# Kernel tuning notes

Hardware: AMD Instinct MI355X
Metric: run time of the kernel (lower is better)

Reference implementation:

```python
import jax, jax.numpy as jnp
import numpy as np
from math import factorial, sqrt

BATCH = 4096
RS_IN = [(16, 0), (16, 1), (16, 2)]   # (mul, l), parity 0
RS_OUT = [(16, 0), (16, 1), (16, 2)]

# selection rule: l_filter in [|l_in-l_out|, l_in+l_out]
SET_LF = sorted({l for (_, li) in RS_IN for (_, lo) in RS_OUT
                 for l in range(abs(li - lo), li + lo + 1)})
Y_OFF = {l: sum(2 * k + 1 for k in SET_LF if k < l) for l in SET_LF}
Y_DIM = sum(2 * l + 1 for l in SET_LF)  # 25


def wigner_3j(j1, j2, j3, m1, m2, m3):
    if m1 + m2 + m3 != 0 or not (abs(j1 - j2) <= j3 <= j1 + j2):
        return 0.0
    if abs(m1) > j1 or abs(m2) > j2 or abs(m3) > j3:
        return 0.0
    f = factorial
    pre = sqrt(f(j1 + j2 - j3) * f(j1 - j2 + j3) * f(-j1 + j2 + j3) / f(j1 + j2 + j3 + 1))
    pre *= sqrt(f(j1 + m1) * f(j1 - m1) * f(j2 + m2) * f(j2 - m2) * f(j3 + m3) * f(j3 - m3))
    s = 0.0
    for t in range(max(0, j2 - j3 - m1, j1 - j3 + m2),
                   min(j1 + j2 - j3, j1 - m1, j2 + m2) + 1):
        s += (-1) ** t / (f(t) * f(j3 - j2 + m1 + t) * f(j3 - j1 - m2 + t)
                          * f(j1 + j2 - j3 - t) * f(j1 - m1 - t) * f(j2 + m2 - t))
    return (-1) ** (j1 - j2 - m3) * pre * s


def real_to_complex(l):
    # A[M+l, m+l]: complex Y^M expressed in the real SH basis
    A = np.zeros((2 * l + 1, 2 * l + 1), dtype=np.complex128)
    A[l, l] = 1.0
    s2 = 1.0 / np.sqrt(2.0)
    for m in range(1, l + 1):
        A[l + m, l + m] = (-1) ** m * s2
        A[l + m, l - m] = 1j * (-1) ** m * s2
        A[l - m, l + m] = s2
        A[l - m, l - m] = -1j * s2
    return A


def clebsch_gordan(l1, l2, l3):
    # real, unit-Frobenius-norm invariant 3-tensor (unique up to sign)
    T = np.zeros((2 * l1 + 1, 2 * l2 + 1, 2 * l3 + 1))
    for m1 in range(-l1, l1 + 1):
        for m2 in range(-l2, l2 + 1):
            m3 = -(m1 + m2)
            if abs(m3) <= l3:
                T[m1 + l1, m2 + l2, m3 + l3] = wigner_3j(l1, l2, l3, m1, m2, m3)
    A1, A2, A3 = real_to_complex(l1), real_to_complex(l2), real_to_complex(l3)
    C = np.einsum('abc,ai,bj,ck->ijk', T, A1.conj(), A2.conj(), A3.conj())
    C = C.real if np.linalg.norm(C.real) >= np.linalg.norm(C.imag) else C.imag
    n = np.linalg.norm(C)
    return (C / n).astype(np.float32) if n > 0 else C.astype(np.float32)


# precompute per-block padded CG tensors and R offsets
R_OFF = {}
C_BLOCKS = {}
_off = 0
for _i, (_mo, _lo) in enumerate(RS_OUT):
    for _j, (_mi, _li) in enumerate(RS_IN):
        _lfs = list(range(abs(_li - _lo), _li + _lo + 1))
        R_OFF[(_i, _j)] = (_off, len(_lfs))
        _off += _mo * _mi * len(_lfs)
        _C = np.zeros((len(_lfs), 2 * _lo + 1, 2 * _li + 1, Y_DIM), dtype=np.float32)
        for _k, _lf in enumerate(_lfs):
            _o = Y_OFF[_lf]
            _C[_k, :, :, _o:_o + 2 * _lf + 1] = clebsch_gordan(_lo, _li, _lf)
        C_BLOCKS[(_i, _j)] = jnp.asarray(_C)
N_PATH = _off  # 4864


def setup_inputs() -> dict:
    key = jax.random.key(0)
    k1, k2, k3 = jax.random.split(key, 3)
    Y = jax.random.normal(k1, (Y_DIM, BATCH), dtype=jnp.float32)
    R = jax.random.normal(k2, (BATCH, N_PATH), dtype=jnp.float32)
    norm_coef = jax.random.uniform(k3, (len(RS_OUT), len(RS_IN), BATCH),
                                   dtype=jnp.float32, minval=0.5, maxval=1.5)
    return {"Y": Y, "R": R, "norm_coef": norm_coef}


def reference(Y, R, norm_coef):
    # Y: [Y_DIM, batch], R: [batch, N_PATH], norm_coef: [3, 3, batch]
    batch = Y.shape[1]
    rows = []
    for i, (mo, lo) in enumerate(RS_OUT):
        row = []
        for j, (mi, li) in enumerate(RS_IN):
            off, nlf = R_OFF[(i, j)]
            sub_R = R[:, off:off + mo * mi * nlf].reshape(batch, mo, mi, nlf)
            # fuse the per-l_filter loop into one contraction over k and m
            K = jnp.einsum('kijm,mz,zuvk,z->zuivj',
                           C_BLOCKS[(i, j)], Y, sub_R, norm_coef[i, j])
            row.append(K.reshape(batch, mo * (2 * lo + 1), mi * (2 * li + 1)))
        rows.append(jnp.concatenate(row, axis=2))
    return jnp.concatenate(rows, axis=1)  # [batch, 144, 144]
```

## Files before the change

kernel.cpp:

```cpp
#include <hip/hip_runtime.h>

#define NPATH 4864
#define YDIM  25
#define NW    259
#define NCG   1225


struct Tables {
    float cg[NCG];
    int   woff[NW];
    int   wlf[NW];
    int   wij[NW];
};

constexpr double cfact(int n) { double f = 1.0; for (int i = 2; i <= n; ++i) f *= (double)i; return f; }

constexpr double csqrt_(double x) {
    if (x <= 0.0) return 0.0;
    double g = x > 1.0 ? x : 1.0, p = 0.0;
    for (int it = 0; it < 200; ++it) { p = g; g = 0.5 * (g + x / g); if (g == p) break; }
    return g;
}
constexpr int cabs_(int x) { return x < 0 ? -x : x; }
constexpr int cmax3(int a, int b, int c) { int m = a > b ? a : b; return m > c ? m : c; }
constexpr int cmin3(int a, int b, int c) { int m = a < b ? a : b; return m < c ? m : c; }

constexpr double cwig3j(int j1, int j2, int j3, int m1, int m2, int m3) {
    if (m1 + m2 + m3 != 0) return 0.0;
    if (cabs_(m1) > j1 || cabs_(m2) > j2 || cabs_(m3) > j3) return 0.0;
    if (j3 < cabs_(j1 - j2) || j3 > j1 + j2) return 0.0;
    double prod = cfact(j1 + j2 - j3) * cfact(j1 - j2 + j3) * cfact(-j1 + j2 + j3)
                / cfact(j1 + j2 + j3 + 1);
    prod *= cfact(j1 + m1) * cfact(j1 - m1) * cfact(j2 + m2) * cfact(j2 - m2)
          * cfact(j3 + m3) * cfact(j3 - m3);
    double pre = csqrt_(prod);
    int t0 = cmax3(0, j2 - j3 - m1, j1 - j3 + m2);
    int t1 = cmin3(j1 + j2 - j3, j1 - m1, j2 + m2);
    double s = 0.0;
    for (int t = t0; t <= t1; ++t) {
        double d = cfact(t) * cfact(j3 - j2 + m1 + t) * cfact(j3 - j1 - m2 + t)
                 * cfact(j1 + j2 - j3 - t) * cfact(j1 - m1 - t) * cfact(j2 + m2 - t);
        s += ((t & 1) ? -1.0 : 1.0) / d;
    }
    int p = j1 - j2 - m3; p = ((p % 2) + 2) % 2;
    return (p ? -1.0 : 1.0) * pre * s;
}

struct Ent { int col; double re; double im; };

constexpr int arow(int l, int a, Ent* e) {
    int m = a - l;
    double s2 = csqrt_(0.5);
    if (m == 0) { e[0] = Ent{l, 1.0, 0.0}; return 1; }
    if (m > 0) {
        double sgn = (m & 1) ? -1.0 : 1.0;
        e[0] = Ent{l + m, sgn * s2, 0.0};
        e[1] = Ent{l - m, 0.0, sgn * s2};
        return 2;
    }
    int mm = -m;
    e[0] = Ent{l + mm, s2, 0.0};
    e[1] = Ent{l - mm, 0.0, -s2};
    return 2;
}

constexpr Tables make_tables() {
    Tables T{};
    const int CL1[19]  = {0,0,0,1,1,1,1,1,1,1,2,2,2,2,2,2,2,2,2};
    const int CL2[19]  = {0,1,2,0,1,1,1,2,2,2,0,1,1,1,2,2,2,2,2};
    const int CL3[19]  = {0,1,2,1,0,1,2,1,2,3,2,1,2,3,0,1,2,3,4};
    const int COFF[19] = {0,1,10,35,44,53,80,125,170,245,350,375,420,495,600,625,700,825,1000};

    for (int c = 0; c < 19; ++c) {
        int l1 = CL1[c], l2 = CL2[c], l3 = CL3[c], coff = COFF[c];
        int n1 = 2 * l1 + 1, n2 = 2 * l2 + 1, n3 = 2 * l3 + 1, ntot = n1 * n2 * n3;
        double Cre[225] = {}, Cim[225] = {};
        for (int a = 0; a < n1; ++a)
            for (int b = 0; b < n2; ++b) {
                int m1 = a - l1, m2 = b - l2, m3 = -(m1 + m2);
                if (cabs_(m3) > l3) continue;
                double tv = cwig3j(l1, l2, l3, m1, m2, m3);
                if (tv == 0.0) continue;
                int crow = m3 + l3;
                Ent e1[2] = {}, e2[2] = {}, e3[2] = {};
                int k1 = arow(l1, a, e1), k2 = arow(l2, b, e2), k3 = arow(l3, crow, e3);
                for (int x = 0; x < k1; ++x)
                    for (int y = 0; y < k2; ++y)
                        for (int w = 0; w < k3; ++w) {
                            double r1 = e1[x].re, i1 = -e1[x].im;
                            double r2 = e2[y].re, i2 = -e2[y].im;
                            double r3 = e3[w].re, i3 = -e3[w].im;
                            double pr = r1 * r2 - i1 * i2, pi = r1 * i2 + i1 * r2;
                            double qr = pr * r3 - pi * i3, qi = pr * i3 + pi * r3;
                            int idx = (e1[x].col * n2 + e2[y].col) * n3 + e3[w].col;
                            Cre[idx] += tv * qr;
                            Cim[idx] += tv * qi;
                        }
            }
        double sR = 0.0, sI = 0.0;
        for (int i = 0; i < ntot; ++i) { sR += Cre[i] * Cre[i]; sI += Cim[i] * Cim[i]; }
        bool useRe = (sR >= sI);
        double nn = csqrt_(useRe ? sR : sI);
        double inv = nn > 0.0 ? 1.0 / nn : 0.0;
        for (int i = 0; i < ntot; ++i)
            T.cg[coff + i] = (float)((useRe ? Cre[i] : Cim[i]) * inv);
    }

    const int NLFt[9]   = {1,1,1,1,3,3,1,3,5};
    const int CGOFF9[9] = {0,1,10,35,44,125,350,375,600};
    int w = 0;
    for (int ij = 0; ij < 9; ++ij) {
        int lo = ij / 3, li = ij % 3;
        int lfmin = lo > li ? lo - li : li - lo;
        int no2 = 2 * lo + 1, ni2 = 2 * li + 1, cgo = CGOFF9[ij];
        for (int k = 0; k < NLFt[ij]; ++k) {
            int lf = lfmin + k;
            for (int a = 0; a < no2; ++a)
                for (int b = 0; b < ni2; ++b) {
                    T.woff[w] = cgo + (a * ni2 + b) * (2 * lf + 1);
                    T.wlf[w]  = lf;
                    T.wij[w]  = ij;
                    ++w;
                }
            cgo += no2 * ni2 * (2 * lf + 1);
        }
    }
    return T;
}

constexpr Tables H_TAB = make_tables();
__device__ __constant__ Tables d_tab = H_TAB;

template <int I, int J, int NLF, int NCQ, int S,
          int WBASE, int ROFF, int ROWB, int COLB>
__device__ __forceinline__ void region(const float* __restrict__ Wl,
                                       const float* __restrict__ Rl,
                                       float* __restrict__ Oz, int t) {
    constexpr int NO2 = 2 * I + 1, NI2 = 2 * J + 1;
    constexpr int NT  = NCQ * NO2 * S;
    constexpr int UL  = 16 / S;
    if (t >= NT) return;

    int c  = t % NCQ;
    int a  = (t / NCQ) % NO2;
    int us = t / (NCQ * NO2);

    float Wreg[NLF][4];
    int rb[4];
#pragma unroll
    for (int cc = 0; cc < 4; ++cc) {
        int cl = 4 * c + cc;
        int v  = cl / NI2;
        int b  = cl - v * NI2;
        rb[cc] = ROFF + v * NLF;
#pragma unroll
        for (int k = 0; k < NLF; ++k)
            Wreg[k][cc] = Wl[WBASE + (k * NO2 + a) * NI2 + b];
    }

    float* obase = Oz + (ROWB + a) * 144 + COLB + 4 * c;
#pragma unroll
    for (int uu = 0; uu < UL; ++uu) {
        int u   = us * UL + uu;
        int rbu = u * 16 * NLF;
        float acc0 = 0.f, acc1 = 0.f, acc2 = 0.f, acc3 = 0.f;
#pragma unroll
        for (int k = 0; k < NLF; ++k) {
            acc0 += Wreg[k][0] * Rl[rb[0] + rbu + k];
            acc1 += Wreg[k][1] * Rl[rb[1] + rbu + k];
            acc2 += Wreg[k][2] * Rl[rb[2] + rbu + k];
            acc3 += Wreg[k][3] * Rl[rb[3] + rbu + k];
        }
        *(float4*)(obase + u * NO2 * 144) = make_float4(acc0, acc1, acc2, acc3);
    }
}


__global__ __launch_bounds__(256) void tp_kernel(const float* __restrict__ Yg,
                                                 const float* __restrict__ Rg,
                                                 const float* __restrict__ Ng,
                                                 float* __restrict__ Og, int batch) {
    __shared__ __align__(16) float Rl[NPATH];
    __shared__ float Wl[NW];
    __shared__ float Ys[YDIM];
    __shared__ float Ns[9];

    int z = blockIdx.x;
    int t = threadIdx.x;

    const float4* Rg4 = (const float4*)(Rg + (size_t)z * NPATH);
    float4* Rl4 = (float4*)Rl;
    for (int p = t; p < NPATH / 4; p += 256) Rl4[p] = Rg4[p];
    if (t < YDIM) Ys[t] = Yg[t * batch + z];
    if (t >= 32 && t < 41) Ns[t - 32] = Ng[(t - 32) * batch + z];
    __syncthreads();

    for (int w = t; w < NW; w += 256) {
        int off = d_tab.woff[w], lf = d_tab.wlf[w];
        float acc = 0.f;
        for (int ci = 0; ci <= 2 * lf; ++ci) acc += d_tab.cg[off + ci] * Ys[lf * lf + ci];
        Wl[w] = acc * Ns[d_tab.wij[w]];
    }
    __syncthreads();

    float* Oz = Og + (size_t)z * 20736;

    region<2, 2, 5, 20, 2, 134, 3584, 64, 64>(Wl, Rl, Oz, t);
    region<2, 1, 3, 12, 4,  89, 2816, 64, 16>(Wl, Rl, Oz, t);
    region<1, 2, 3, 20, 4,  39, 1792, 16, 64>(Wl, Rl, Oz, t);
    region<1, 1, 3, 12, 4,  12, 1024, 16, 16>(Wl, Rl, Oz, t);
    region<2, 0, 1,  4, 8,  84, 2560, 64,  0>(Wl, Rl, Oz, t);
    region<0, 2, 1, 20, 8,   4,  512,  0, 64>(Wl, Rl, Oz, t);
    region<1, 0, 1,  4,16,   9,  768, 16,  0>(Wl, Rl, Oz, t);
    region<0, 1, 1, 12,16,   1,  256,  0, 16>(Wl, Rl, Oz, t);
    region<0, 0, 1,  4,16,   0,    0,  0,  0>(Wl, Rl, Oz, t);
}

extern "C" void kernel_launch(void* const* d_in, const int* in_sizes, int n_in,
                              void* d_out, int out_size, void* d_ws, size_t ws_size,
                              hipStream_t stream) {
    const float* Y = (const float*)d_in[0];
    const float* R = (const float*)d_in[1];
    const float* N = (const float*)d_in[2];
    float* O = (float*)d_out;
    int batch = in_sizes[0] / YDIM;

    hipLaunchKernelGGL(tp_kernel, dim3(batch), dim3(256), 0, stream, Y, R, N, O, batch);
}
```

Before: 429.1 us.

## Remap threads to (u,v) channel pairs with padded broadcast weight layout

Each thread now owns one (output channel u, input channel v) pair across all nine blocks. It loads its R path coefficients once into registers and reads the per-block CG-filter weights as padded, vectorized broadcast LDS loads. The weight table is scattered into a padded layout so rows can be read as float4. This removes the per-thread weight gathers and the per-region idle threads, but output stores become scalar and strided (NI2 wide per thread) instead of float4-coalesced, which may hurt global write efficiency.

```diff
diff --git a/kernel.cpp b/kernel.cpp
--- a/kernel.cpp
+++ b/kernel.cpp
@@ -4,6 +4,7 @@
 #define YDIM  25
 #define NW    259
 #define NCG   1225
+#define NWP   400
 
 
 struct Tables {
@@ -11,6 +12,7 @@
     int   woff[NW];
     int   wlf[NW];
     int   wij[NW];
+    int   wdst[NW];
 };
 
 constexpr double cfact(int n) { double f = 1.0; for (int i = 2; i <= n; ++i) f *= (double)i; return f; }
@@ -108,6 +110,8 @@
 
     const int NLFt[9]   = {1,1,1,1,3,3,1,3,5};
     const int CGOFF9[9] = {0,1,10,35,44,125,350,375,600};
+    const int WPB[9]  = {0, 4, 8, 16, 20, 56, 128, 136, 200};
+    const int PADt[9] = {1, 4, 8,  1,  4,  8,   1,   4,   8};
     int w = 0;
     for (int ij = 0; ij < 9; ++ij) {
         int lo = ij / 3, li = ij % 3;
@@ -120,6 +124,7 @@
                     T.woff[w] = cgo + (a * ni2 + b) * (2 * lf + 1);
                     T.wlf[w]  = lf;
                     T.wij[w]  = ij;
+                    T.wdst[w] = WPB[ij] + (k * no2 + a) * PADt[ij] + b;
                     ++w;
                 }
             cgo += no2 * ni2 * (2 * lf + 1);
@@ -131,48 +136,50 @@
 constexpr Tables H_TAB = make_tables();
 __device__ __constant__ Tables d_tab = H_TAB;
 
-template <int I, int J, int NLF, int NCQ, int S,
-          int WBASE, int ROFF, int ROWB, int COLB>
-__device__ __forceinline__ void region(const float* __restrict__ Wl,
+template <int I, int J, int NLF, int WPB, int PAD, int ROFF, int ROWB, int COLB>
+__device__ __forceinline__ void region(const float* __restrict__ Wp,
                                        const float* __restrict__ Rl,
-                                       float* __restrict__ Oz, int t) {
+                                       float* __restrict__ Oz, int u, int v) {
     constexpr int NO2 = 2 * I + 1, NI2 = 2 * J + 1;
-    constexpr int NT  = NCQ * NO2 * S;
-    constexpr int UL  = 16 / S;
-    if (t >= NT) return;
-
-    int c  = t % NCQ;
-    int a  = (t / NCQ) % NO2;
-    int us = t / (NCQ * NO2);
-
-    float Wreg[NLF][4];
-    int rb[4];
-#pragma unroll
-    for (int cc = 0; cc < 4; ++cc) {
-        int cl = 4 * c + cc;
-        int v  = cl / NI2;
-        int b  = cl - v * NI2;
-        rb[cc] = ROFF + v * NLF;
-#pragma unroll
-        for (int k = 0; k < NLF; ++k)
-            Wreg[k][cc] = Wl[WBASE + (k * NO2 + a) * NI2 + b];
-    }
-
-    float* obase = Oz + (ROWB + a) * 144 + COLB + 4 * c;
-#pragma unroll
-    for (int uu = 0; uu < UL; ++uu) {
-        int u   = us * UL + uu;
-        int rbu = u * 16 * NLF;
-        float acc0 = 0.f, acc1 = 0.f, acc2 = 0.f, acc3 = 0.f;
-#pragma unroll
-        for (int k = 0; k < NLF; ++k) {
-            acc0 += Wreg[k][0] * Rl[rb[0] + rbu + k];
-            acc1 += Wreg[k][1] * Rl[rb[1] + rbu + k];
-            acc2 += Wreg[k][2] * Rl[rb[2] + rbu + k];
-            acc3 += Wreg[k][3] * Rl[rb[3] + rbu + k];
+    const float* rb = Rl + ROFF + (u * 16 + v) * NLF;
+    float Rk[NLF];
+#pragma unroll
+    for (int k = 0; k < NLF; ++k) Rk[k] = rb[k];
+
+    float acc[NO2][NI2];
+#pragma unroll
+    for (int a = 0; a < NO2; ++a)
+#pragma unroll
+        for (int b = 0; b < NI2; ++b) acc[a][b] = 0.f;
+
+#pragma unroll
+    for (int k = 0; k < NLF; ++k)
+#pragma unroll
+        for (int a = 0; a < NO2; ++a) {
+            const float* wrow = Wp + WPB + (k * NO2 + a) * PAD;
+            if constexpr (NI2 == 1) {
+                acc[a][0] += wrow[0] * Rk[k];
+            } else if constexpr (NI2 == 3) {
+                float4 w4 = *(const float4*)wrow;
+                acc[a][0] += w4.x * Rk[k];
+                acc[a][1] += w4.y * Rk[k];
+                acc[a][2] += w4.z * Rk[k];
+            } else {
+                float4 w4 = *(const float4*)wrow;
+                float  w5 = wrow[4];
+                acc[a][0] += w4.x * Rk[k];
+                acc[a][1] += w4.y * Rk[k];
+                acc[a][2] += w4.z * Rk[k];
+                acc[a][3] += w4.w * Rk[k];
+                acc[a][4] += w5   * Rk[k];
+            }
         }
-        *(float4*)(obase + u * NO2 * 144) = make_float4(acc0, acc1, acc2, acc3);
-    }
+
+    float* ob = Oz + (ROWB + u * NO2) * 144 + COLB + v * NI2;
+#pragma unroll
+    for (int a = 0; a < NO2; ++a)
+#pragma unroll
+        for (int b = 0; b < NI2; ++b) ob[a * 144 + b] = acc[a][b];
 }
 
 
@@ -181,7 +188,7 @@
                                                  const float* __restrict__ Ng,
                                                  float* __restrict__ Og, int batch) {
     __shared__ __align__(16) float Rl[NPATH];
-    __shared__ float Wl[NW];
+    __shared__ __align__(16) float Wp[NWP];
     __shared__ float Ys[YDIM];
     __shared__ float Ns[9];
 
@@ -199,21 +206,22 @@
         int off = d_tab.woff[w], lf = d_tab.wlf[w];
         float acc = 0.f;
         for (int ci = 0; ci <= 2 * lf; ++ci) acc += d_tab.cg[off + ci] * Ys[lf * lf + ci];
-        Wl[w] = acc * Ns[d_tab.wij[w]];
+        Wp[d_tab.wdst[w]] = acc * Ns[d_tab.wij[w]];
     }
     __syncthreads();
 
     float* Oz = Og + (size_t)z * 20736;
-
-    region<2, 2, 5, 20, 2, 134, 3584, 64, 64>(Wl, Rl, Oz, t);
-    region<2, 1, 3, 12, 4,  89, 2816, 64, 16>(Wl, Rl, Oz, t);
-    region<1, 2, 3, 20, 4,  39, 1792, 16, 64>(Wl, Rl, Oz, t);
-    region<1, 1, 3, 12, 4,  12, 1024, 16, 16>(Wl, Rl, Oz, t);
-    region<2, 0, 1,  4, 8,  84, 2560, 64,  0>(Wl, Rl, Oz, t);
-    region<0, 2, 1, 20, 8,   4,  512,  0, 64>(Wl, Rl, Oz, t);
-    region<1, 0, 1,  4,16,   9,  768, 16,  0>(Wl, Rl, Oz, t);
-    region<0, 1, 1, 12,16,   1,  256,  0, 16>(Wl, Rl, Oz, t);
-    region<0, 0, 1,  4,16,   0,    0,  0,  0>(Wl, Rl, Oz, t);
+    int u = t >> 4, v = t & 15;
+
+    region<0, 0, 1,   0, 1,     0,  0,  0>(Wp, Rl, Oz, u, v);
+    region<0, 1, 1,   4, 4,   256,  0, 16>(Wp, Rl, Oz, u, v);
+    region<0, 2, 1,   8, 8,   512,  0, 64>(Wp, Rl, Oz, u, v);
+    region<1, 0, 1,  16, 1,   768, 16,  0>(Wp, Rl, Oz, u, v);
+    region<1, 1, 3,  20, 4,  1024, 16, 16>(Wp, Rl, Oz, u, v);
+    region<1, 2, 3,  56, 8,  1792, 16, 64>(Wp, Rl, Oz, u, v);
+    region<2, 0, 1, 128, 1,  2560, 64,  0>(Wp, Rl, Oz, u, v);
+    region<2, 1, 3, 136, 4,  2816, 64, 16>(Wp, Rl, Oz, u, v);
+    region<2, 2, 5, 200, 8,  3584, 64, 64>(Wp, Rl, Oz, u, v);
 }
 
 extern "C" void kernel_launch(void* const* d_in, const int* in_sizes, int n_in,
```

Measured after the change: 417.1 us. -2.8%, faster.
